# Kernel tuning notes

Hardware: AMD Instinct MI355X
Metric: run time of the kernel (lower is better)

The kernel has to match this reference:

```python
import jax, jax.numpy as jnp
import numpy as np

B, S, D, G = 16, 2048, 768, 1024  # batch, max_len, embedding_dim, groups per row (pairs)


def setup_inputs() -> dict:
    key = jax.random.key(0)
    k1, k2, k3, k4 = jax.random.split(key, 4)
    tensors_batch = jax.random.normal(k1, (B, S, D), jnp.float32)
    # ragged chunk structure encoded densely: token j belongs to group j//2 (contiguous pairs)
    group_ids = jnp.tile(jnp.arange(S, dtype=jnp.int32) // 2, (B, 1))
    padding_mask = jnp.ones((B, S), jnp.int32)  # all tokens real -> no column removal
    # masks must be constant within each group (the module asserts any()==all())
    regular_tokens_mask = jnp.repeat(jax.random.randint(k2, (B, G), 0, 2, jnp.int32), 2, axis=1)
    seq_pair_mask = jnp.repeat(jax.random.randint(k3, (B, G), 0, 2, jnp.int32), 2, axis=1)
    W = jax.random.normal(k4, (D, D), jnp.float32) / np.sqrt(D)
    b = jnp.zeros((D,), jnp.float32)
    return {
        "tensors_batch": tensors_batch,
        "group_ids": group_ids,
        "padding_mask": padding_mask,
        "regular_tokens_mask": regular_tokens_mask,
        "seq_pair_mask": seq_pair_mask,
        "num_groups": G,
        "W": W,
        "b": b,
    }


def reference(tensors_batch, group_ids, padding_mask, regular_tokens_mask, seq_pair_mask, num_groups, W, b):
    Bv, Sv, Dv = tensors_batch.shape
    Gv = num_groups
    # flatten (batch, group) into one segment axis: segment id = b*G + group
    flat_ids = (group_ids + jnp.arange(Bv, dtype=group_ids.dtype)[:, None] * Gv).reshape(-1)
    # gen_net = mean over group tokens, then Linear + tanh (applied to every group at once)
    sums = jax.ops.segment_sum(tensors_batch.reshape(Bv * Sv, Dv), flat_ids, num_segments=Bv * Gv)
    counts = jax.ops.segment_sum(jnp.ones((Bv * Sv,), tensors_batch.dtype), flat_ids, num_segments=Bv * Gv)
    mean = sums / counts[:, None]
    compact = jnp.tanh(mean @ W + b).reshape(Bv, Gv, Dv)
    # per-group mask reductions (masks are group-constant by construction)
    seg_any = lambda m: (jax.ops.segment_max(m.reshape(-1), flat_ids, num_segments=Bv * Gv) > 0)
    seg_all = lambda m: (jax.ops.segment_min(m.reshape(-1), flat_ids, num_segments=Bv * Gv) > 0)
    mask_padding = seg_any(padding_mask).astype(jnp.int32).reshape(Bv, Gv)        # sum != 0
    mask_regular = seg_any(regular_tokens_mask).astype(jnp.int32).reshape(Bv, Gv) # sum != 0
    mask_seq_pair = seg_all(seq_pair_mask).astype(jnp.int32).reshape(Bv, Gv)      # prod != 0
    mask_seq_pair = jnp.where(mask_padding == 0, jnp.int32(-1), mask_seq_pair)
    # column removal: keep columns where any batch has a real group; with all-real padding
    # every column is kept, so shapes stay static (faithful to original under these inputs)
    compression_rate = mask_regular.sum().astype(jnp.float32) / regular_tokens_mask.sum().astype(jnp.float32)
    return compact, mask_padding, mask_regular, mask_seq_pair, compression_rate
```

## Files before the change

kernel.cpp:

```cpp
#include <hip/hip_runtime.h>
#include <hip/hip_bf16.h>

#define NB 16
#define NS 2048
#define ND 768
#define NG 1024
#define ROWS (NB * NG)

#define BM 64
#define BN 256
#define BK 32
#define NCOL (ND / BN)
#define NROW (ROWS / BM)

typedef __attribute__((ext_vector_type(8))) __bf16 bf16x8;
typedef __attribute__((ext_vector_type(8))) unsigned short ushort8_t;
typedef __attribute__((ext_vector_type(4))) float f32x4;

__device__ __forceinline__ unsigned short f2bf(float f) {
    unsigned int u = __builtin_bit_cast(unsigned int, f);
    return (unsigned short)((u + 0x7FFFu + ((u >> 16) & 1u)) >> 16);
}

__device__ __forceinline__ void gload_lds16(const void* g, void* l) {
    __builtin_amdgcn_global_load_lds((const __attribute__((address_space(1))) unsigned int*)g,
                                     (__attribute__((address_space(3))) unsigned int*)l, 16, 0, 0);
}

__device__ __forceinline__ float fast_tanh(float v) {
    float x = fminf(fmaxf(v, -15.f), 15.f);
    float e = __expf(2.f * x);
    return (e - 1.f) / (e + 1.f);
}

__global__ __launch_bounds__(256) void wtrans_kernel(const float* __restrict__ W,
                                                     unsigned short* __restrict__ Bt) {
    __shared__ float tile[64][65];
    int n0 = blockIdx.x * 64;
    int k0 = blockIdx.y * 64;
    int tx = threadIdx.x & 63;
    int ty = threadIdx.x >> 6;
    #pragma unroll
    for (int i = 0; i < 64; i += 4)
        tile[ty + i][tx] = W[(long)(k0 + ty + i) * ND + n0 + tx];
    __syncthreads();
    #pragma unroll
    for (int i = 0; i < 64; i += 4)
        Bt[(long)(n0 + ty + i) * ND + k0 + tx] = f2bf(0.5f * tile[tx][ty + i]);
}

__global__ __launch_bounds__(256, 3) void gemm_fused_kernel(const float* __restrict__ x,
                                                            const unsigned short* __restrict__ Bt,
                                                            const float* __restrict__ bias,
                                                            float* __restrict__ out) {
    __shared__ unsigned short Al[BM * BK];
    __shared__ unsigned short Bl[BN * BK];
    int tid = threadIdx.x;
    int lane = tid & 63;
    int w = tid >> 6;
    int wr = w >> 1, wc = w & 1;

    int bid = blockIdx.x;
    int xcd = bid & 7;
    int s = bid >> 3;
    int c = s % 3;
    int rb = (s / 3) * 8 + xcd;
    int row0 = rb * BM;
    int col0 = c * BN;
    int r = lane & 15, h = lane >> 4;

    int b = row0 >> 10;
    long tokrow = (long)b * NS + 2 * (row0 & (NG - 1));

    const float* ax0 = x + (tokrow + 2 * (tid >> 2)) * ND + (tid & 3) * 8;
    const float* ax1 = ax0 + ND;
    char* alw = (char*)Al + tid * 16;

    const char* gB = (const char*)Bt + (long)(col0 + (tid >> 2)) * (ND * 2) + (tid & 3) * 16;
    char* lB = (char*)Bl + tid * 16;

    float4 a0[2], a1[2];
    #pragma unroll
    for (int j = 0; j < 2; ++j) {
        a0[j] = *(const float4*)(ax0 + j * 4);
        a1[j] = *(const float4*)(ax1 + j * 4);
    }

    f32x4 acc[2][8] = {};

    for (int k0 = 0; k0 < ND; k0 += BK) {
        ushort8_t aw;
        #pragma unroll
        for (int e = 0; e < 4; ++e) {
            aw[e]     = f2bf(a0[0][e] + a1[0][e]);
            aw[4 + e] = f2bf(a0[1][e] + a1[1][e]);
        }
        *(ushort8_t*)alw = aw;
        #pragma unroll
        for (int q = 0; q < 4; ++q)
            gload_lds16(gB + (long)q * 64 * (ND * 2), lB + q * 4096);
        gB += BK * 2;
        __syncthreads();

        int adv = (k0 + BK < ND) ? BK : 0;
        ax0 += adv; ax1 += adv;
        #pragma unroll
        for (int j = 0; j < 2; ++j) {
            a0[j] = *(const float4*)(ax0 + j * 4);
            a1[j] = *(const float4*)(ax1 + j * 4);
        }

        bf16x8 af[2];
        #pragma unroll
        for (int m = 0; m < 2; ++m)
            af[m] = __builtin_bit_cast(bf16x8, *(const ushort8_t*)&Al[(wr * 32 + m * 16 + r) * BK + h * 8]);
        #pragma unroll
        for (int n = 0; n < 8; ++n) {
            bf16x8 bfv = __builtin_bit_cast(bf16x8, *(const ushort8_t*)&Bl[(wc * 128 + n * 16 + r) * BK + h * 8]);
            #pragma unroll
            for (int m = 0; m < 2; ++m)
                acc[m][n] = __builtin_amdgcn_mfma_f32_16x16x32_bf16(af[m], bfv, acc[m][n], 0, 0, 0);
        }
        __syncthreads();
    }

    float bv[8];
    #pragma unroll
    for (int n = 0; n < 8; ++n) bv[n] = bias[col0 + wc * 128 + n * 16 + r];

    #pragma unroll
    for (int m = 0; m < 2; ++m) {
        #pragma unroll
        for (int q = 0; q < 4; ++q) {
            int orow = row0 + wr * 32 + m * 16 + h * 4 + q;
            float* op = out + (long)orow * ND + col0 + wc * 128 + r;
            #pragma unroll
            for (int n = 0; n < 8; ++n)
                op[n * 16] = fast_tanh(acc[m][n][q] + bv[n]);
        }
    }
}

__global__ __launch_bounds__(256) void masks_kernel(const int* __restrict__ padding,
                                                    const int* __restrict__ regular,
                                                    const int* __restrict__ seqpair,
                                                    float* __restrict__ out_mp,
                                                    float* __restrict__ out_mr,
                                                    float* __restrict__ out_ms,
                                                    int2* __restrict__ partials) {
    int i = blockIdx.x * 256 + threadIdx.x;
    int b = i >> 10, g = i & (NG - 1);
    int t = b * NS + 2 * g;
    int r0 = regular[t], r1 = regular[t + 1];
    int p  = ((padding[t] | padding[t + 1]) != 0) ? 1 : 0;
    int mr = ((r0 | r1) != 0) ? 1 : 0;
    int ms = ((seqpair[t] > 0) && (seqpair[t + 1] > 0)) ? 1 : 0;
    if (p == 0) ms = -1;
    out_mp[i] = (float)p;
    out_mr[i] = (float)mr;
    out_ms[i] = (float)ms;

    int mrs = mr, tok = r0 + r1;
    #pragma unroll
    for (int off = 32; off > 0; off >>= 1) {
        mrs += __shfl_down(mrs, off);
        tok += __shfl_down(tok, off);
    }
    __shared__ int sm[4], st[4];
    int wv = threadIdx.x >> 6, lane = threadIdx.x & 63;
    if (lane == 0) { sm[wv] = mrs; st[wv] = tok; }
    __syncthreads();
    if (threadIdx.x == 0)
        partials[blockIdx.x] = make_int2(sm[0] + sm[1] + sm[2] + sm[3],
                                         st[0] + st[1] + st[2] + st[3]);
}

__global__ void cr_kernel(const int2* __restrict__ partials, float* __restrict__ cr) {
    int2 p = partials[threadIdx.x];
    int a = p.x, t = p.y;
    #pragma unroll
    for (int off = 32; off > 0; off >>= 1) {
        a += __shfl_down(a, off);
        t += __shfl_down(t, off);
    }
    if (threadIdx.x == 0) cr[0] = (float)a / (float)t;
}

extern "C" void kernel_launch(void* const* d_in, const int* in_sizes, int n_in,
                              void* d_out, int out_size, void* d_ws, size_t ws_size,
                              hipStream_t stream) {
    const float* x        = (const float*)d_in[0];
    const int*   padding  = (const int*)d_in[2];
    const int*   regular  = (const int*)d_in[3];
    const int*   seqpair  = (const int*)d_in[4];
    const float* W        = (const float*)d_in[6];
    const float* bias     = (const float*)d_in[7];

    float* outc   = (float*)d_out;
    float* out_mp = outc + (long)ROWS * ND;
    float* out_mr = out_mp + ROWS;
    float* out_ms = out_mr + ROWS;
    float* out_cr = out_ms + ROWS;

    unsigned short* wbt = (unsigned short*)d_ws;
    int2* partials = (int2*)((char*)d_ws + 1179648);

    wtrans_kernel<<<dim3(ND / 64, ND / 64), 256, 0, stream>>>(W, wbt);
    masks_kernel<<<ROWS / 256, 256, 0, stream>>>(padding, regular, seqpair, out_mp, out_mr, out_ms, partials);
    gemm_fused_kernel<<<NCOL * NROW, 256, 0, stream>>>(x, wbt, bias, outc);
    cr_kernel<<<1, 64, 0, stream>>>(partials, out_cr);
}
```

Baseline: 206.6 us.

## Reorder LDS tile layout to fragment order and switch to 1x4 warp split

The A and B tiles are now written into LDS in the exact order that MFMA fragments are read, so each lane reads a contiguous 16 bytes at lane*16 and bank conflicts from the old row-strided reads go away. The warp tiling changes from 2x2 (32x128 per warp) to 1x4 (64x64 per warp), which alters the ratio of fragment loads to MFMAs. The B prefetch into LDS is also issued before the A conversion and store. The risk is that global load coalescing changes, since each lane now reads from a strided row/column mapping.

```diff
diff --git a/kernel.cpp b/kernel.cpp
--- a/kernel.cpp
+++ b/kernel.cpp
@@ -58,7 +58,7 @@
     int tid = threadIdx.x;
     int lane = tid & 63;
     int w = tid >> 6;
-    int wr = w >> 1, wc = w & 1;
+    int r = lane & 15, h = lane >> 4;
 
     int bid = blockIdx.x;
     int xcd = bid & 7;
@@ -67,75 +67,68 @@
     int rb = (s / 3) * 8 + xcd;
     int row0 = rb * BM;
     int col0 = c * BN;
-    int r = lane & 15, h = lane >> 4;
 
     int b = row0 >> 10;
     long tokrow = (long)b * NS + 2 * (row0 & (NG - 1));
 
-    const float* ax0 = x + (tokrow + 2 * (tid >> 2)) * ND + (tid & 3) * 8;
+    int ag = w * 16 + r;
+    const float* ax0 = x + (tokrow + 2 * ag) * ND + h * 8;
     const float* ax1 = ax0 + ND;
     char* alw = (char*)Al + tid * 16;
 
-    const char* gB = (const char*)Bt + (long)(col0 + (tid >> 2)) * (ND * 2) + (tid & 3) * 16;
+    const char* gBbase = (const char*)Bt + (long)(col0 + w * 16 + r) * (ND * 2) + h * 16;
     char* lB = (char*)Bl + tid * 16;
 
-    float4 a0[2], a1[2];
-    #pragma unroll
-    for (int j = 0; j < 2; ++j) {
-        a0[j] = *(const float4*)(ax0 + j * 4);
-        a1[j] = *(const float4*)(ax1 + j * 4);
-    }
-
-    f32x4 acc[2][8] = {};
+    float4 a0, a1, b0, b1;
+    a0 = *(const float4*)ax0;  b0 = *(const float4*)(ax0 + 4);
+    a1 = *(const float4*)ax1;  b1 = *(const float4*)(ax1 + 4);
+
+    f32x4 acc[4][4] = {};
 
     for (int k0 = 0; k0 < ND; k0 += BK) {
+        #pragma unroll
+        for (int q = 0; q < 4; ++q)
+            gload_lds16(gBbase + (long)q * 64 * (ND * 2) + k0 * 2, lB + q * 4096);
         ushort8_t aw;
         #pragma unroll
         for (int e = 0; e < 4; ++e) {
-            aw[e]     = f2bf(a0[0][e] + a1[0][e]);
-            aw[4 + e] = f2bf(a0[1][e] + a1[1][e]);
+            aw[e]     = f2bf(a0[e] + a1[e]);
+            aw[4 + e] = f2bf(b0[e] + b1[e]);
         }
         *(ushort8_t*)alw = aw;
-        #pragma unroll
-        for (int q = 0; q < 4; ++q)
-            gload_lds16(gB + (long)q * 64 * (ND * 2), lB + q * 4096);
-        gB += BK * 2;
         __syncthreads();
 
         int adv = (k0 + BK < ND) ? BK : 0;
         ax0 += adv; ax1 += adv;
-        #pragma unroll
-        for (int j = 0; j < 2; ++j) {
-            a0[j] = *(const float4*)(ax0 + j * 4);
-            a1[j] = *(const float4*)(ax1 + j * 4);
-        }
-
-        bf16x8 af[2];
-        #pragma unroll
-        for (int m = 0; m < 2; ++m)
-            af[m] = __builtin_bit_cast(bf16x8, *(const ushort8_t*)&Al[(wr * 32 + m * 16 + r) * BK + h * 8]);
-        #pragma unroll
-        for (int n = 0; n < 8; ++n) {
-            bf16x8 bfv = __builtin_bit_cast(bf16x8, *(const ushort8_t*)&Bl[(wc * 128 + n * 16 + r) * BK + h * 8]);
+        a0 = *(const float4*)ax0;  b0 = *(const float4*)(ax0 + 4);
+        a1 = *(const float4*)ax1;  b1 = *(const float4*)(ax1 + 4);
+
+        bf16x8 af[4];
+        #pragma unroll
+        for (int m = 0; m < 4; ++m)
+            af[m] = __builtin_bit_cast(bf16x8, *(const ushort8_t*)((const char*)Al + m * 1024 + lane * 16));
+        #pragma unroll
+        for (int n = 0; n < 4; ++n) {
+            bf16x8 bfv = __builtin_bit_cast(bf16x8, *(const ushort8_t*)((const char*)Bl + (w * 4 + n) * 1024 + lane * 16));
             #pragma unroll
-            for (int m = 0; m < 2; ++m)
+            for (int m = 0; m < 4; ++m)
                 acc[m][n] = __builtin_amdgcn_mfma_f32_16x16x32_bf16(af[m], bfv, acc[m][n], 0, 0, 0);
         }
         __syncthreads();
     }
 
-    float bv[8];
-    #pragma unroll
-    for (int n = 0; n < 8; ++n) bv[n] = bias[col0 + wc * 128 + n * 16 + r];
-
-    #pragma unroll
-    for (int m = 0; m < 2; ++m) {
+    float bv[4];
+    #pragma unroll
+    for (int n = 0; n < 4; ++n) bv[n] = bias[col0 + w * 64 + n * 16 + r];
+
+    #pragma unroll
+    for (int m = 0; m < 4; ++m) {
         #pragma unroll
         for (int q = 0; q < 4; ++q) {
-            int orow = row0 + wr * 32 + m * 16 + h * 4 + q;
-            float* op = out + (long)orow * ND + col0 + wc * 128 + r;
+            int orow = row0 + m * 16 + h * 4 + q;
+            float* op = out + (long)orow * ND + col0 + w * 64 + r;
             #pragma unroll
-            for (int n = 0; n < 8; ++n)
+            for (int n = 0; n < 4; ++n)
                 op[n * 16] = fast_tanh(acc[m][n][q] + bv[n]);
         }
     }
```

Result: slower. 230.5 us (+11.6%).
